# Kernel tuning notes

Measured on AMD Instinct MI355X. Metric: run time of the kernel, lower is better.

## Reference

```python
import jax, jax.numpy as jnp
import numpy as np

THRESH = 1e-5   # replace_denormals threshold
EPS = 1e-5      # instance_norm eps

NUM_LAYERS, TOKEN_LEN, EMBED = 24, 100, 1024
N, B = 1025, 8  # seq (incl. cls token), batch


def _replace_denormals(x):
    return jnp.where((x < THRESH) & (x > -THRESH), THRESH, x)


def _delta_feat(feats, tokens, w_t2f, b_t2f, w_df, b_df, instance_norm):
    # feats: [n, b, c], tokens: [m, c]
    attn = jnp.einsum('nbc,mc->nbm', feats, tokens)
    if instance_norm:  # normalize over m per (n, b), biased variance (torch F.instance_norm)
        mu = attn.mean(axis=-1, keepdims=True)
        var = attn.var(axis=-1, keepdims=True)
        attn = (attn - mu) / jnp.sqrt(var + EPS)
    attn = jax.nn.softmax(attn * (feats.shape[-1] ** -0.5), axis=-1)
    v = tokens[1:] @ w_t2f.T + b_t2f                     # [m-1, c]
    df = jnp.einsum('nbm,mc->nbc', attn[:, :, 1:], v)    # drop first token column
    return (df + feats) @ w_df.T + b_df


def setup_inputs() -> dict:
    key = jax.random.key(0)
    ks = jax.random.split(key, 12)
    C = EMBED
    inp = {
        'feats': jax.random.normal(ks[0], (N, B, C), dtype=jnp.float32),
        'learnable_tokens': jax.random.normal(ks[1], (NUM_LAYERS, TOKEN_LEN, C), dtype=jnp.float32) * 0.04,
        'learnable_tokens2': jax.random.normal(ks[2], (NUM_LAYERS, TOKEN_LEN, C), dtype=jnp.float32) * 0.04,
        'w_t2f': jax.random.normal(ks[3], (C, C), dtype=jnp.float32) * 0.02,
        'b_t2f': jax.random.normal(ks[4], (C,), dtype=jnp.float32) * 0.02,
        'w_df': jax.random.normal(ks[5], (C, C), dtype=jnp.float32) * 0.02,
        'b_df': jax.random.normal(ks[6], (C,), dtype=jnp.float32) * 0.02,
        'w_t2f2': jax.random.normal(ks[7], (C, C), dtype=jnp.float32) * 0.02,
        'b_t2f2': jax.random.normal(ks[8], (C,), dtype=jnp.float32) * 0.02,
        'w_df2': jax.random.normal(ks[9], (C, C), dtype=jnp.float32) * 0.02,
        'b_df2': jax.random.normal(ks[10], (C,), dtype=jnp.float32) * 0.02,
        'scale': jnp.float32(0.001),
        'layer': 0,
    }
    return inp


def reference(feats, learnable_tokens, learnable_tokens2,
              w_t2f, b_t2f, w_df, b_df,
              w_t2f2, b_t2f2, w_df2, b_df2,
              scale, layer):
    # batch_first=False, has_cls_token=True (defaults)
    C = feats.shape[-1]
    cls_tok, x = feats[:1], feats[1:]            # [1,b,c], [n,b,c]
    n, b = x.shape[0], x.shape[1]

    # decompose: fft2 over last two dims (b, c), norm='backward'
    f = jnp.fft.fft2(x)
    re, im = jnp.real(f), jnp.imag(f)
    amp = jnp.sqrt(_replace_denormals(re * re + im * im))
    phase = jnp.arctan2(im, _replace_denormals(re))

    t1 = learnable_tokens[layer]
    t2 = learnable_tokens2[layer]
    d_phase = _delta_feat(phase, t1, w_t2f, b_t2f, w_df, b_df, instance_norm=False)
    d_amp = _delta_feat(amp, t2, w_t2f2, b_t2f2, w_df2, b_df2, instance_norm=True)

    # compose: stacked last dim has size 2, dim 2 has size C -> divide by sqrt(C*2)
    z = (jnp.cos(d_phase) * d_amp + 1j * (jnp.sin(d_phase) * d_amp)) / np.float32(np.sqrt(C * 2.0))
    z = z[..., : C // 2 + 1]                      # torch irfft2 trims last dim to s[-1]//2+1
    delta = jnp.fft.irfft2(z, s=(b, C), norm='ortho')

    out = x + delta * scale
    return jnp.concatenate([cls_tok, out], axis=0)
```

## Files before the change

### kernel.cpp

```cpp
#include <hip/hip_runtime.h>
#include <cstddef>


using bf16x8 = __attribute__((ext_vector_type(8))) short;
using f32x4  = __attribute__((ext_vector_type(4))) float;

__device__ inline short f2bf(float f) {
  union { float f; unsigned u; } v; v.f = f;
  unsigned r = v.u + 0x7FFFu + ((v.u >> 16) & 1u);
  return (short)(r >> 16);
}
__device__ inline float bf2f(short s) {
  union { unsigned u; float f; } v; v.u = ((unsigned)(unsigned short)s) << 16;
  return v.f;
}
__device__ inline void async16(const void* g, void* l) {
  __builtin_amdgcn_global_load_lds(
      (const __attribute__((address_space(1))) void*)g,
      (__attribute__((address_space(3))) void*)l, 16, 0, 0);
}
__device__ inline float fast_atan2(float y, float x) {
  float ax = fabsf(x), ay = fabsf(y);
  float mx = fmaxf(ax, ay), mn = fminf(ax, ay);
  float a = mn * __frcp_rn(mx);
  float s = a * a;
  float r = fmaf(fmaf(fmaf(-0.0464964749f, s, 0.15931422f), s, -0.327622764f),
                 s * a, a);
  if (ay > ax) r = 1.5707963267948966f - r;
  if (x < 0.f) r = 3.14159265358979f - r;
  return (y < 0.f) ? -r : r;
}

__device__ inline int PADi(int i) { return i + (i >> 5); }
__device__ inline int rev4_8(int t) {
  return ((t & 3) << 6) | (((t >> 2) & 3) << 4) | (((t >> 4) & 3) << 2) | ((t >> 6) & 3);
}

__device__ inline void fft8_fwd(float* xr, float* xi) {
  const float r = 0.70710678118654752f;
  float ar[4], ai[4], br[4], bi[4], tr, ti;
  ar[0]=xr[0]+xr[4]; ai[0]=xi[0]+xi[4]; br[0]=xr[0]-xr[4]; bi[0]=xi[0]-xi[4];
  ar[1]=xr[1]+xr[5]; ai[1]=xi[1]+xi[5];
  tr=xr[1]-xr[5]; ti=xi[1]-xi[5]; br[1]=(tr+ti)*r; bi[1]=(ti-tr)*r;
  ar[2]=xr[2]+xr[6]; ai[2]=xi[2]+xi[6];
  tr=xr[2]-xr[6]; ti=xi[2]-xi[6]; br[2]=ti; bi[2]=-tr;
  ar[3]=xr[3]+xr[7]; ai[3]=xi[3]+xi[7];
  tr=xr[3]-xr[7]; ti=xi[3]-xi[7]; br[3]=(ti-tr)*r; bi[3]=-(tr+ti)*r;
  float u0r=ar[0]+ar[2], u0i=ai[0]+ai[2], u1r=ar[1]+ar[3], u1i=ai[1]+ai[3];
  float v0r=ar[0]-ar[2], v0i=ai[0]-ai[2];
  tr=ar[1]-ar[3]; ti=ai[1]-ai[3];
  float v1r=ti, v1i=-tr;
  xr[0]=u0r+u1r; xi[0]=u0i+u1i; xr[4]=u0r-u1r; xi[4]=u0i-u1i;
  xr[2]=v0r+v1r; xi[2]=v0i+v1i; xr[6]=v0r-v1r; xi[6]=v0i-v1i;
  u0r=br[0]+br[2]; u0i=bi[0]+bi[2]; u1r=br[1]+br[3]; u1i=bi[1]+bi[3];
  v0r=br[0]-br[2]; v0i=bi[0]-bi[2];
  tr=br[1]-br[3]; ti=bi[1]-bi[3];
  v1r=ti; v1i=-tr;
  xr[1]=u0r+u1r; xi[1]=u0i+u1i; xr[5]=u0r-u1r; xi[5]=u0i-u1i;
  xr[3]=v0r+v1r; xi[3]=v0i+v1i; xr[7]=v0r-v1r; xi[7]=v0i-v1i;
}
__device__ inline void fft8_inv(float* xr, float* xi) {
  const float r = 0.70710678118654752f;
  float ar[4], ai[4], br[4], bi[4], tr, ti;
  ar[0]=xr[0]+xr[4]; ai[0]=xi[0]+xi[4]; br[0]=xr[0]-xr[4]; bi[0]=xi[0]-xi[4];
  ar[1]=xr[1]+xr[5]; ai[1]=xi[1]+xi[5];
  tr=xr[1]-xr[5]; ti=xi[1]-xi[5]; br[1]=(tr-ti)*r; bi[1]=(tr+ti)*r;
  ar[2]=xr[2]+xr[6]; ai[2]=xi[2]+xi[6];
  tr=xr[2]-xr[6]; ti=xi[2]-xi[6]; br[2]=-ti; bi[2]=tr;
  ar[3]=xr[3]+xr[7]; ai[3]=xi[3]+xi[7];
  tr=xr[3]-xr[7]; ti=xi[3]-xi[7]; br[3]=-(tr+ti)*r; bi[3]=(tr-ti)*r;
  float u0r=ar[0]+ar[2], u0i=ai[0]+ai[2], u1r=ar[1]+ar[3], u1i=ai[1]+ai[3];
  float v0r=ar[0]-ar[2], v0i=ai[0]-ai[2];
  tr=ar[1]-ar[3]; ti=ai[1]-ai[3];
  float v1r=-ti, v1i=tr;
  xr[0]=u0r+u1r; xi[0]=u0i+u1i; xr[4]=u0r-u1r; xi[4]=u0i-u1i;
  xr[2]=v0r+v1r; xi[2]=v0i+v1i; xr[6]=v0r-v1r; xi[6]=v0i-v1i;
  u0r=br[0]+br[2]; u0i=bi[0]+bi[2]; u1r=br[1]+br[3]; u1i=bi[1]+bi[3];
  v0r=br[0]-br[2]; v0i=bi[0]-bi[2];
  tr=br[1]-br[3]; ti=bi[1]-bi[3];
  v1r=-ti; v1i=tr;
  xr[1]=u0r+u1r; xi[1]=u0i+u1i; xr[5]=u0r-u1r; xi[5]=u0i-u1i;
  xr[3]=v0r+v1r; xi[3]=v0i+v1i; xr[7]=v0r-v1r; xi[7]=v0i-v1i;
}

template <int SIGN, int NP>
__device__ inline void fft1024xN(float2 (*zb)[1056], int t) {
#pragma unroll
  for (int s = 0; s < 5; ++s) {
    const int Q = 256 >> (2 * s);
    const int j = t & (Q - 1);
    const int i0 = ((t & ~(Q - 1)) << 2) + j;
    const float ang = (float)SIGN * 6.283185307179586f * (float)j / (float)(4 * Q);
    float s1, c1; __sincosf(ang, &s1, &c1);
    const float c2 = c1 * c1 - s1 * s1, s2 = 2.f * c1 * s1;
    const float c3 = c2 * c1 - s2 * s1, s3 = c2 * s1 + s2 * c1;
#pragma unroll
    for (int p = 0; p < NP; ++p) {
      float2* z = zb[p];
      float2 x0 = z[PADi(i0)];
      float2 x1 = z[PADi(i0 + Q)];
      float2 x2 = z[PADi(i0 + 2 * Q)];
      float2 x3 = z[PADi(i0 + 3 * Q)];
      float t0x = x0.x + x2.x, t0y = x0.y + x2.y;
      float t1x = x0.x - x2.x, t1y = x0.y - x2.y;
      float t2x = x1.x + x3.x, t2y = x1.y + x3.y;
      float t3x = x1.x - x3.x, t3y = x1.y - x3.y;
      float u0x = t0x + t2x, u0y = t0y + t2y;
      float u2x = t0x - t2x, u2y = t0y - t2y;
      float u1x, u1y, u3x, u3y;
      if (SIGN < 0) { u1x = t1x + t3y; u1y = t1y - t3x; u3x = t1x - t3y; u3y = t1y + t3x; }
      else          { u1x = t1x - t3y; u1y = t1y + t3x; u3x = t1x + t3y; u3y = t1y - t3x; }
      z[PADi(i0)]         = make_float2(u0x, u0y);
      z[PADi(i0 + Q)]     = make_float2(u1x * c1 - u1y * s1, u1x * s1 + u1y * c1);
      z[PADi(i0 + 2 * Q)] = make_float2(u2x * c2 - u2y * s2, u2x * s2 + u2y * c2);
      z[PADi(i0 + 3 * Q)] = make_float2(u3x * c3 - u3y * s3, u3x * s3 + u3y * c3);
    }
    __syncthreads();
  }
}

__global__ __launch_bounds__(256) void fwd_fft2_amp_conv(
    const float* __restrict__ feats,
    short* __restrict__ ampb, short* __restrict__ phaseb,
    const float* __restrict__ w1, const float* __restrict__ w2,
    const float* __restrict__ w3, const float* __restrict__ w4,
    const float* __restrict__ lt1, const float* __restrict__ lt2,
    const int* __restrict__ layerp,
    short* __restrict__ Wdst, short* __restrict__ Tdst,
    float* __restrict__ out) {
  if (blockIdx.x >= 1024) {
    const int id = blockIdx.x - 1024;
    const int t4 = threadIdx.x * 4;
    if (id < 4096) {
      const int z = id >> 10, row = id & 1023;
      const float* W = (z == 0 ? w1 : z == 1 ? w2 : z == 2 ? w3 : w4)
                       + (size_t)row * 1024;
      short* D = Wdst + ((size_t)z * 1024 + row) * 1024;
      float4 v = *(const float4*)(W + t4);
      D[t4] = f2bf(v.x); D[t4 + 1] = f2bf(v.y); D[t4 + 2] = f2bf(v.z); D[t4 + 3] = f2bf(v.w);
    } else if (id < 4608) {
      const int i2 = id - 4096;
      const int zz = i2 >> 7, row = i2 & 127;
      const int z = zz & 1, shift = zz >> 1;
      short* D = Tdst + ((size_t)zz * 128 + row) * 1024;
      if (row + shift < 100) {
        const float* S = (z ? lt2 : lt1) + (size_t)layerp[0] * 102400
                         + (size_t)(row + shift) * 1024;
        float4 v = *(const float4*)(S + t4);
        D[t4] = f2bf(v.x); D[t4 + 1] = f2bf(v.y); D[t4 + 2] = f2bf(v.z); D[t4 + 3] = f2bf(v.w);
      } else {
        D[t4] = 0; D[t4 + 1] = 0; D[t4 + 2] = 0; D[t4 + 3] = 0;
      }
    } else {
      const int i = (id - 4608) * 256 + threadIdx.x;
      out[i] = feats[i];
    }
    return;
  }
  __shared__ float2 zb[4][1056];
  const int t = threadIdx.x;
  const int n = blockIdx.x;
  const float* base = feats + 8192 + (size_t)n * 8192;
#pragma unroll
  for (int p = 0; p < 4; ++p) {
    const float* x0 = base + (size_t)(2 * p) * 1024;
    const float* x1 = x0 + 1024;
#pragma unroll
    for (int m = 0; m < 4; ++m) {
      const int c = t + 256 * m;
      zb[p][PADi(c)] = make_float2(x0[c], x1[c]);
    }
  }
  __syncthreads();
  fft1024xN<-1, 4>(zb, t);
  const int rt = rev4_8(t);
  short* ab = ampb + (size_t)n * 8192;
  short* pb = phaseb + (size_t)n * 8192;
#pragma unroll
  for (int m = 0; m < 4; ++m) {
    const int k = 256 * m + t;
    const int kk = (1024 - k) & 1023;
    const int pos  = 4 * rt + m;
    const int pos2 = 4 * rev4_8(kk & 255) + (kk >> 8);
    float xr[8], xi[8];
#pragma unroll
    for (int p = 0; p < 4; ++p) {
      float2 Z = zb[p][PADi(pos)];
      float2 W = zb[p][PADi(pos2)];
      xr[2 * p]     = 0.5f * (Z.x + W.x);
      xi[2 * p]     = 0.5f * (Z.y - W.y);
      xr[2 * p + 1] = 0.5f * (Z.y + W.y);
      xi[2 * p + 1] = 0.5f * (W.x - Z.x);
    }
    fft8_fwd(xr, xi);
#pragma unroll
    for (int kb = 0; kb < 8; ++kb) {
      float sr = xr[kb], si = xi[kb];
      float r2 = sr * sr + si * si;
      if (r2 < 1e-5f) r2 = 1e-5f;
      float a = sqrtf(r2);
      float rr = (sr < 1e-5f && sr > -1e-5f) ? 1e-5f : sr;
      float ph = fast_atan2(si, rr);
      ab[kb * 1024 + k] = f2bf(a);
      pb[kb * 1024 + k] = f2bf(ph);
    }
  }
}

__global__ __launch_bounds__(256) void gemm_sm_v(
    const short* A0, const short* A1,
    const short* Tok,
    const short* Wall,
    const float* bt1, const float* bt2,
    short* __restrict__ awb,
    short* __restrict__ vrow) {
  __shared__ __align__(16) char smem[39040];
  const int z = blockIdx.z;
  const int tid = threadIdx.x;
  const int wave = tid >> 6, lane = tid & 63;
  const int m16 = lane & 15, quad = lane >> 4;
  const int fcol = ((quad ^ ((m16 >> 1) & 3)) * 8) + m16 * 32;
  const int r0 = tid >> 2;
  const int csw = (((tid & 3) ^ ((r0 >> 1) & 3)) * 8);

  if (blockIdx.x >= 256) {
    const int jb = blockIdx.x - 256;
    const short* A = Tok + (size_t)(2 + z) * 128 * 1024;
    const short* B = Wall + (size_t)z * 1024 * 1024;
    const float* bias = z ? bt2 : bt1;
    short* C = vrow + (size_t)z * 128 * 1024;
    const int K = 1024;
    short* As = (short*)smem;
    short* Bs = (short*)(smem + 8192);
    const int wm = (wave & 1) * 64, wn = (wave >> 1) * 64;
    f32x4 acc[4][4];
#pragma unroll
    for (int i = 0; i < 4; ++i)
#pragma unroll
      for (int j = 0; j < 4; ++j) acc[i][j] = (f32x4){0.f, 0.f, 0.f, 0.f};
    const short* aSrc0 = A + (size_t)r0 * K + csw;
    const short* aSrc1 = aSrc0 + (size_t)64 * K;
    const short* bSrc0 = B + (size_t)(jb * 128 + r0) * K + csw;
    const short* bSrc1 = bSrc0 + (size_t)64 * K;
    short* aDst0 = As + tid * 8;
    short* aDst1 = As + 2048 + tid * 8;
    short* bDst0 = Bs + tid * 8;
    short* bDst1 = Bs + 2048 + tid * 8;
    for (int k0 = 0; k0 < K; k0 += 32) {
      async16(aSrc0 + k0, aDst0);
      async16(aSrc1 + k0, aDst1);
      async16(bSrc0 + k0, bDst0);
      async16(bSrc1 + k0, bDst1);
      __syncthreads();
      bf16x8 af[4], bg[4];
#pragma unroll
      for (int ib = 0; ib < 4; ++ib)
        af[ib] = *(const bf16x8*)(As + (wm + ib * 16) * 32 + fcol);
#pragma unroll
      for (int jb2 = 0; jb2 < 4; ++jb2)
        bg[jb2] = *(const bf16x8*)(Bs + (wn + jb2 * 16) * 32 + fcol);
#pragma unroll
      for (int ib = 0; ib < 4; ++ib)
#pragma unroll
        for (int jb2 = 0; jb2 < 4; ++jb2)
          acc[ib][jb2] = __builtin_amdgcn_mfma_f32_16x16x32_bf16(af[ib], bg[jb2], acc[ib][jb2], 0, 0, 0);
      __syncthreads();
    }
#pragma unroll
    for (int ib = 0; ib < 4; ++ib) {
      const int rowb = wm + ib * 16 + quad * 4;
#pragma unroll
      for (int jb2 = 0; jb2 < 4; ++jb2) {
        const int col = jb * 128 + wn + jb2 * 16 + m16;
        const float bcv = bias[col];
#pragma unroll
        for (int r = 0; r < 4; ++r)
          C[(size_t)(rowb + r) * 1024 + col] = f2bf(acc[ib][jb2][r] + bcv);
      }
    }
    return;
  }

  const short* A = z ? A1 : A0;
  const short* B = Tok + (size_t)z * 128 * 1024;
  const int K = 1024;
  short* As = (short*)smem;
  short* Bs = (short*)(smem + 4096);
  float (*ltile)[129] = (float(*)[129])(smem + 20480);
  float (*red1)[8] = (float(*)[8])(smem + 36992);
  float (*red2)[8] = (float(*)[8])(smem + 38016);
  const int wm = (wave & 1) * 16, wn = (wave >> 1) * 64;
  f32x4 acc[4];
#pragma unroll
  for (int j = 0; j < 4; ++j) acc[j] = (f32x4){0.f, 0.f, 0.f, 0.f};
  const int asub = tid >> 7, aidx = tid & 127;
  const int ar0 = aidx >> 2;
  const int acsw = (((aidx & 3) ^ ((ar0 >> 1) & 3)) * 8);
  const short* aSrc = A + (size_t)(blockIdx.x * 32 + ar0) * K + acsw + asub * 32;
  short* aDst = As + asub * 1024 + aidx * 8;
  const short* bSrc0 = B + (size_t)r0 * K + csw;
  const short* bSrc1 = bSrc0 + (size_t)64 * K;
  short* bDst00 = Bs + tid * 8;
  short* bDst01 = Bs + 2048 + tid * 8;
  short* bDst10 = Bs + 4096 + tid * 8;
  short* bDst11 = Bs + 4096 + 2048 + tid * 8;
  for (int k0 = 0; k0 < K; k0 += 64) {
    async16(aSrc + k0, aDst);
    async16(bSrc0 + k0, bDst00);
    async16(bSrc1 + k0, bDst01);
    async16(bSrc0 + k0 + 32, bDst10);
    async16(bSrc1 + k0 + 32, bDst11);
    __syncthreads();
#pragma unroll
    for (int sub = 0; sub < 2; ++sub) {
      bf16x8 af = *(const bf16x8*)(As + sub * 1024 + wm * 32 + fcol);
      bf16x8 bg[4];
#pragma unroll
      for (int jb = 0; jb < 4; ++jb)
        bg[jb] = *(const bf16x8*)(Bs + sub * 4096 + (wn + jb * 16) * 32 + fcol);
#pragma unroll
      for (int jb = 0; jb < 4; ++jb)
        acc[jb] = __builtin_amdgcn_mfma_f32_16x16x32_bf16(af, bg[jb], acc[jb], 0, 0, 0);
    }
    __syncthreads();
  }
#pragma unroll
  for (int jb = 0; jb < 4; ++jb)
#pragma unroll
    for (int r = 0; r < 4; ++r)
      ltile[wm + quad * 4 + r][wn + jb * 16 + m16] = acc[jb][r];
  __syncthreads();
  const int row = tid >> 3, l8 = tid & 7;
  float s = 0.f, q = 0.f;
  for (int c = l8; c < 100; c += 8) { float x = ltile[row][c]; s += x; q += x * x; }
  red1[row][l8] = s; red2[row][l8] = q;
  __syncthreads();
  float ssum = 0.f, qsum = 0.f;
#pragma unroll
  for (int i = 0; i < 8; ++i) { ssum += red1[row][i]; qsum += red2[row][i]; }
  __syncthreads();
  const float mu = ssum * 0.01f;
  const float rinv = rsqrtf(fmaxf(qsum * 0.01f - mu * mu, 0.f) + 1e-5f);
  float mx = -3.4e38f;
  for (int c = l8; c < 100; c += 8) {
    float x = ltile[row][c];
    if (z == 1) x = (x - mu) * rinv;
    x *= 0.03125f;
    ltile[row][c] = x;
    mx = fmaxf(mx, x);
  }
  red1[row][l8] = mx;
  __syncthreads();
#pragma unroll
  for (int i = 0; i < 8; ++i) mx = fmaxf(mx, red1[row][i]);
  __syncthreads();
  float es = 0.f;
  for (int c = l8; c < 100; c += 8) {
    float e = __expf(ltile[row][c] - mx);
    ltile[row][c] = e; es += e;
  }
  red1[row][l8] = es;
  __syncthreads();
  float tot = 0.f;
#pragma unroll
  for (int i = 0; i < 8; ++i) tot += red1[row][i];
  const float inv = 1.f / tot;
  short* Aout = awb + ((size_t)z * 8192 + (size_t)blockIdx.x * 32 + row) * 128;
  for (int c = l8; c < 100; c += 8)
    if (c >= 1) Aout[c - 1] = f2bf(ltile[row][c] * inv);
  for (int k = l8; k < 128; k += 8)
    if (k >= 99) Aout[k] = 0;
}

__global__ __launch_bounds__(256) void gemm64(
    const short* A0, const short* A1,
    const short* B0, const short* B1,
    void* C0v, void* C1v, int K, int ldc) {
  const int z = blockIdx.z;
  const short* A = z ? A1 : A0;
  const short* B = z ? B1 : B0;
  void* Cv = z ? C1v : C0v;
  __shared__ __align__(16) short As[64 * 32];
  __shared__ __align__(16) short Bs[128 * 32];
  const int tid = threadIdx.x;
  const int wave = tid >> 6, lane = tid & 63;
  const int m16 = lane & 15, quad = lane >> 4;
  const int wm = (wave & 1) * 32, wn = (wave >> 1) * 64;
  f32x4 acc[2][4];
#pragma unroll
  for (int i = 0; i < 2; ++i)
#pragma unroll
    for (int j = 0; j < 4; ++j) acc[i][j] = (f32x4){0.f, 0.f, 0.f, 0.f};
  const int r0 = tid >> 2;
  const int csw = (((tid & 3) ^ ((r0 >> 1) & 3)) * 8);
  const short* aSrc  = A + (size_t)(blockIdx.x * 64 + r0) * K + csw;
  const short* bSrc0 = B + (size_t)r0 * K + csw;
  const short* bSrc1 = bSrc0 + (size_t)64 * K;
  short* aDst  = As + tid * 8;
  short* bDst0 = Bs + tid * 8;
  short* bDst1 = Bs + 2048 + tid * 8;
  const int fcol = ((quad ^ ((m16 >> 1) & 3)) * 8) + m16 * 32;
  for (int k0 = 0; k0 < K; k0 += 32) {
    async16(aSrc + k0, aDst);
    async16(bSrc0 + k0, bDst0);
    async16(bSrc1 + k0, bDst1);
    __syncthreads();
    bf16x8 af[2], bg[4];
#pragma unroll
    for (int ib = 0; ib < 2; ++ib)
      af[ib] = *(const bf16x8*)(As + (wm + ib * 16) * 32 + fcol);
#pragma unroll
    for (int jb = 0; jb < 4; ++jb)
      bg[jb] = *(const bf16x8*)(Bs + (wn + jb * 16) * 32 + fcol);
#pragma unroll
    for (int ib = 0; ib < 2; ++ib)
#pragma unroll
      for (int jb = 0; jb < 4; ++jb)
        acc[ib][jb] = __builtin_amdgcn_mfma_f32_16x16x32_bf16(af[ib], bg[jb], acc[ib][jb], 0, 0, 0);
    __syncthreads();
  }
#pragma unroll
  for (int ib = 0; ib < 2; ++ib) {
    const int rowb = blockIdx.x * 64 + wm + ib * 16 + quad * 4;
#pragma unroll
    for (int jb = 0; jb < 4; ++jb) {
      const int col = wn + jb * 16 + m16;
#pragma unroll
      for (int r = 0; r < 4; ++r)
        ((short*)Cv)[(size_t)(rowb + r) * ldc + col] = f2bf(acc[ib][jb][r]);
    }
  }
}

#define DUAL_STEP(VM, DOISS)                                                 \
  do {                                                                       \
    asm volatile("s_waitcnt vmcnt(" #VM ")" ::: "memory");                   \
    __builtin_amdgcn_s_barrier();                                            \
    if (DOISS) {                                                             \
      const int kp = k + 3;                                                  \
      short* ad = &As[kp & 3][0];                                            \
      short* bd = &Bs[kp & 3][0];                                            \
      const short *as0, *as1, *bs0, *bs1;                                    \
      if (kp < NS1) {                                                        \
        const int c = kp << 5;                                               \
        as0 = A1 + aO1_0 + c; as1 = A1 + aO1_1 + c;                          \
        bs0 = B1 + bO1_0 + c; bs1 = B1 + bO1_1 + c;                          \
      } else {                                                               \
        const int c = (kp - NS1) << 5;                                       \
        as0 = A2 + aO2_0 + c; as1 = A2 + aO2_1 + c;                          \
        bs0 = B2 + bO2_0 + c; bs1 = B2 + bO2_1 + c;                          \
      }                                                                      \
      async16(as0, ad + tid * 8);                                            \
      async16(as1, ad + 4096 + tid * 8);                                     \
      async16(bs0, bd + tid * 8);                                            \
      async16(bs1, bd + 4096 + tid * 8);                                     \
    }                                                                        \
    {                                                                        \
      const short* Asl = &As[k & 3][0];                                      \
      const short* Bsl = &Bs[k & 3][0];                                      \
      bf16x8 bg[4], af[4];                                                   \
      _Pragma("unroll")                                                      \
      for (int jb = 0; jb < 4; ++jb)                                         \
        bg[jb] = *(const bf16x8*)(Bsl + (wn + jb * 16) * 32 + fcol);         \
      _Pragma("unroll")                                                      \
      for (int ib = 0; ib < 4; ++ib)                                         \
        af[ib] = *(const bf16x8*)(Asl + (wm + ib * 16) * 32 + fcol);         \
      _Pragma("unroll")                                                      \
      for (int ib = 0; ib < 4; ++ib)                                         \
        _Pragma("unroll")                                                    \
        for (int jb = 0; jb < 4; ++jb)                                       \
          acc[ib][jb] = __builtin_amdgcn_mfma_f32_16x16x32_bf16(             \
              af[ib], bg[jb], acc[ib][jb], 0, 0, 0);                         \
      _Pragma("unroll")                                                      \
      for (int ib = 0; ib < 4; ++ib)                                         \
        af[ib] = *(const bf16x8*)(Asl + (wm + 64 + ib * 16) * 32 + fcol);    \
      _Pragma("unroll")                                                      \
      for (int ib = 0; ib < 4; ++ib)                                         \
        _Pragma("unroll")                                                    \
        for (int jb = 0; jb < 4; ++jb)                                       \
          acc[ib + 4][jb] = __builtin_amdgcn_mfma_f32_16x16x32_bf16(         \
              af[ib], bg[jb], acc[ib + 4][jb], 0, 0, 0);                     \
    }                                                                        \
    __builtin_amdgcn_sched_barrier(0);                                       \
  } while (0)

__global__ __launch_bounds__(512) void gemm256_dual(
    const short* A1_0, const short* A1_1,
    const short* B1_0, const short* B1_1,
    const short* A2_0, const short* A2_1,
    const short* B2_0, const short* B2_1,
    const float* bias0, const float* bias1,
    short* C0, short* C1, int K1, int K2, int ldc) {
  const int z = blockIdx.z;
  const short* A1 = z ? A1_1 : A1_0;
  const short* B1 = z ? B1_1 : B1_0;
  const short* A2 = z ? A2_1 : A2_0;
  const short* B2 = z ? B2_1 : B2_0;
  const float* bias = z ? bias1 : bias0;
  short* C = z ? C1 : C0;
  __shared__ __align__(16) short As[4][8192];
  __shared__ __align__(16) short Bs[4][8192];
  const int tid = threadIdx.x;
  const int wave = tid >> 6, lane = tid & 63;
  const int m16 = lane & 15, quad = lane >> 4;
  const int wm = (wave & 1) * 128, wn = (wave >> 1) * 64;
  const int fcol = ((quad ^ ((m16 >> 1) & 3)) * 8) + m16 * 32;
  const int r0 = tid >> 2;
  const int csw = (((tid & 3) ^ ((r0 >> 1) & 3)) * 8);
  const size_t aO1_0 = (size_t)(blockIdx.x * 256 + r0) * (size_t)K1 + csw;
  const size_t aO1_1 = aO1_0 + (size_t)128 * K1;
  const size_t bO1_0 = (size_t)(blockIdx.y * 256 + r0) * (size_t)K1 + csw;
  const size_t bO1_1 = bO1_0 + (size_t)128 * K1;
  const size_t aO2_0 = (size_t)(blockIdx.x * 256 + r0) * (size_t)K2 + csw;
  const size_t aO2_1 = aO2_0 + (size_t)128 * K2;
  const size_t bO2_0 = (size_t)(blockIdx.y * 256 + r0) * (size_t)K2 + csw;
  const size_t bO2_1 = bO2_0 + (size_t)128 * K2;
  const int NS1 = K1 >> 5;
  const int NT  = NS1 + (K2 >> 5);
  f32x4 acc[8][4];
#pragma unroll
  for (int i = 0; i < 8; ++i)
#pragma unroll
    for (int j = 0; j < 4; ++j) acc[i][j] = (f32x4){0.f, 0.f, 0.f, 0.f};
#pragma unroll
  for (int k = 0; k < 3; ++k) {
    short* ad = &As[k & 3][0];
    short* bd = &Bs[k & 3][0];
    const short *as0, *as1, *bs0, *bs1;
    if (k < NS1) {
      const int c = k << 5;
      as0 = A1 + aO1_0 + c; as1 = A1 + aO1_1 + c;
      bs0 = B1 + bO1_0 + c; bs1 = B1 + bO1_1 + c;
    } else {
      const int c = (k - NS1) << 5;
      as0 = A2 + aO2_0 + c; as1 = A2 + aO2_1 + c;
      bs0 = B2 + bO2_0 + c; bs1 = B2 + bO2_1 + c;
    }
    async16(as0, ad + tid * 8);
    async16(as1, ad + 4096 + tid * 8);
    async16(bs0, bd + tid * 8);
    async16(bs1, bd + 4096 + tid * 8);
  }
#pragma unroll 1
  for (int k = 0; k < NT - 2; ++k) {
    DUAL_STEP(8, (k + 3 < NT));
  }
  { const int k = NT - 2; DUAL_STEP(4, false); }
  { const int k = NT - 1; DUAL_STEP(0, false); }
#pragma unroll
  for (int ib = 0; ib < 8; ++ib) {
    const int rowb = blockIdx.x * 256 + wm + ib * 16 + quad * 4;
#pragma unroll
    for (int jb = 0; jb < 4; ++jb) {
      const int col = blockIdx.y * 256 + wn + jb * 16 + m16;
      const float bcv = bias[col];
#pragma unroll
      for (int r = 0; r < 4; ++r) {
        const size_t idx = (size_t)(rowb + r) * (size_t)ldc + col;
        C[idx] = f2bf(acc[ib][jb][r] + bcv);
      }
    }
  }
}
#undef DUAL_STEP

__global__ __launch_bounds__(256) void inv_fft2_res(const short* __restrict__ dPb,
                                                    const short* __restrict__ dAb,
                                                    const float* __restrict__ feats,
                                                    const float* __restrict__ scalep,
                                                    float* __restrict__ out) {
  __shared__ float2 zb[2][1056];
  const int t = threadIdx.x;
  const int n = blockIdx.x >> 1, q = blockIdx.x & 1;
  const short* pp = dPb + (size_t)n * 8192;
  const short* ap = dAb + (size_t)n * 8192;
  const float invs = 0.022097086912079608f;
  const float inv8 = 0.35355339059327373f;
  for (int k = t; k < 513; k += 256) {
    float zr[8], zi[8];
#pragma unroll
    for (int b = 0; b < 8; ++b) {
      float p = bf2f(pp[b * 1024 + k]);
      float a = bf2f(ap[b * 1024 + k]) * invs;
      float s, c; __sincosf(p, &s, &c);
      zr[b] = c * a; zi[b] = s * a;
    }
    fft8_inv(zr, zi);
#pragma unroll
    for (int l = 0; l < 2; ++l) {
      const int bp = 4 * q + 2 * l;
      float ax = zr[bp] * inv8,     ay = zi[bp] * inv8;
      float bx = zr[bp + 1] * inv8, by = zi[bp + 1] * inv8;
      zb[l][PADi(k)] = make_float2(ax - by, ay + bx);
      if (k >= 1 && k <= 511)
        zb[l][PADi(1024 - k)] = make_float2(ax + by, bx - ay);
    }
  }
  __syncthreads();
  fft1024xN<1, 2>(zb, t);
  const int rt = rev4_8(t);
  const float s = scalep[0] * 0.03125f;
#pragma unroll
  for (int l = 0; l < 2; ++l) {
    const int p4 = 2 * q + l;
    const size_t ob0 = 8192 + ((size_t)n * 8 + 2 * p4) * 1024;
    const size_t ob1 = ob0 + 1024;
#pragma unroll
    for (int m = 0; m < 4; ++m) {
      const int nn = 256 * m + t;
      float2 y = zb[l][PADi(4 * rt + m)];
      out[ob0 + nn] = feats[ob0 + nn] + y.x * s;
      out[ob1 + nn] = feats[ob1 + nn] + y.y * s;
    }
  }
}

extern "C" void kernel_launch(void* const* d_in, const int* in_sizes, int n_in,
                              void* d_out, int out_size, void* d_ws, size_t ws_size,
                              hipStream_t stream) {
  const float* feats  = (const float*)d_in[0];
  const float* lt1    = (const float*)d_in[1];
  const float* lt2    = (const float*)d_in[2];
  const float* w_t2f  = (const float*)d_in[3];
  const float* b_t2f  = (const float*)d_in[4];
  const float* w_df   = (const float*)d_in[5];
  const float* b_df   = (const float*)d_in[6];
  const float* w_t2f2 = (const float*)d_in[7];
  const float* b_t2f2 = (const float*)d_in[8];
  const float* w_df2  = (const float*)d_in[9];
  const float* b_df2  = (const float*)d_in[10];
  const float* scalep = (const float*)d_in[11];
  const int*   layerp = (const int*)d_in[12];
  float* out = (float*)d_out;
  (void)in_sizes; (void)n_in; (void)out_size; (void)ws_size;

  const size_t SZ = 8192ull * 1024ull;
  short* Pa   = (short*)d_ws;
  short* Pb   = Pa + SZ;
  short* awb  = Pb + SZ;
  short* Tok  = awb + 2ull * 8192 * 128;
  short* Wall = Tok + 4ull * 128 * 1024;
  short* vrow = Wall + 4ull * 1024 * 1024;
  short* V2T  = vrow + 2ull * 128 * 1024;
  short* dP   = V2T + 2ull * 1024 * 128;
  short* dA   = dP + SZ;

  fwd_fft2_amp_conv<<<dim3(5664), dim3(256), 0, stream>>>(
      feats, Pb, Pa, w_t2f, w_t2f2, w_df, w_df2, lt1, lt2, layerp,
      Wall, Tok, out);
  gemm_sm_v<<<dim3(264, 1, 2), dim3(256), 0, stream>>>(
      Pa, Pb, Tok, Wall, b_t2f, b_t2f2, awb, vrow);
  gemm64<<<dim3(16, 1, 2), dim3(256), 0, stream>>>(
      Wall + 2 * 1024 * 1024, Wall + 3 * 1024 * 1024,
      vrow, vrow + 128 * 1024,
      V2T, V2T + 1024 * 128, 1024, 128);
  gemm256_dual<<<dim3(32, 4, 2), dim3(512), 0, stream>>>(
      awb, awb + 8192 * 128, V2T, V2T + 1024 * 128,
      Pa, Pb, Wall + 2 * 1024 * 1024, Wall + 3 * 1024 * 1024,
      b_df, b_df2, dP, dA, 128, 1024, 1024);
  inv_fft2_res<<<dim3(2048), dim3(256), 0, stream>>>(dP, dA, feats, scalep, out);
}
```

Baseline: 256.8 us.

## Restructure dual GEMM main loop into ping-pong phases with setprio and split loads

The 256x256 dual GEMM K-loop is reorganized into two phases per K-step. Each phase issues LDS fragment reads and half of the async global->LDS prefetches, then hits a barrier and runs a prioritized MFMA block bracketed by s_setprio. The vmcnt wait moves to the end of each step and the loop peeling is adjusted. The aim is to interleave memory issue with MFMA work across waves, in exchange for extra barriers per step and a riskier wait-count schedule.

New measurement: 255.1 us. Within noise of the previous version (-0.7%).

```diff
diff --git a/kernel.cpp b/kernel.cpp
--- a/kernel.cpp
+++ b/kernel.cpp
@@ -432,15 +432,15 @@
   }
 }
 
-#define DUAL_STEP(VM, DOISS)                                                 \
+#define SLOT8(VM, DOSTAGE)                                                   \
   do {                                                                       \
-    asm volatile("s_waitcnt vmcnt(" #VM ")" ::: "memory");                   \
-    __builtin_amdgcn_s_barrier();                                            \
-    if (DOISS) {                                                             \
-      const int kp = k + 3;                                                  \
-      short* ad = &As[kp & 3][0];                                            \
-      short* bd = &Bs[kp & 3][0];                                            \
-      const short *as0, *as1, *bs0, *bs1;                                    \
+    const short* Asl = &As[k & 3][0];                                        \
+    const short* Bsl = &Bs[k & 3][0];                                        \
+    const int kp = k + 3;                                                    \
+    const short *as0 = nullptr, *as1 = nullptr, *bs0 = nullptr, *bs1 = nullptr; \
+    short *ad = nullptr, *bd = nullptr;                                      \
+    if (DOSTAGE) {                                                           \
+      ad = &As[kp & 3][0]; bd = &Bs[kp & 3][0];                              \
       if (kp < NS1) {                                                        \
         const int c = kp << 5;                                               \
         as0 = A1 + aO1_0 + c; as1 = A1 + aO1_1 + c;                          \
@@ -450,38 +450,54 @@
         as0 = A2 + aO2_0 + c; as1 = A2 + aO2_1 + c;                          \
         bs0 = B2 + bO2_0 + c; bs1 = B2 + bO2_1 + c;                          \
       }                                                                      \
+    }                                                                        \
+    bf16x8 bg[4], af[4];                                                     \
+       \
+    _Pragma("unroll")                                                        \
+    for (int jb = 0; jb < 4; ++jb)                                           \
+      bg[jb] = *(const bf16x8*)(Bsl + (wn + jb * 16) * 32 + fcol);           \
+    _Pragma("unroll")                                                        \
+    for (int ib = 0; ib < 4; ++ib)                                           \
+      af[ib] = *(const bf16x8*)(Asl + (wm + ib * 16) * 32 + fcol);           \
+    if (DOSTAGE) {                                                           \
       async16(as0, ad + tid * 8);                                            \
       async16(as1, ad + 4096 + tid * 8);                                     \
+    }                                                                        \
+    __builtin_amdgcn_sched_barrier(0);                                       \
+    __builtin_amdgcn_s_barrier();                                            \
+    asm volatile("s_waitcnt lgkmcnt(0)" ::: "memory");                       \
+    __builtin_amdgcn_s_setprio(1);                                           \
+    _Pragma("unroll")                                                        \
+    for (int ib = 0; ib < 4; ++ib)                                           \
+      _Pragma("unroll")                                                      \
+      for (int jb = 0; jb < 4; ++jb)                                         \
+        acc[ib][jb] = __builtin_amdgcn_mfma_f32_16x16x32_bf16(               \
+            af[ib], bg[jb], acc[ib][jb], 0, 0, 0);                           \
+    __builtin_amdgcn_s_setprio(0);                                           \
+    __builtin_amdgcn_sched_barrier(0);                                       \
+    __builtin_amdgcn_s_barrier();                                            \
+        \
+    _Pragma("unroll")                                                        \
+    for (int ib = 0; ib < 4; ++ib)                                           \
+      af[ib] = *(const bf16x8*)(Asl + (wm + 64 + ib * 16) * 32 + fcol);      \
+    if (DOSTAGE) {                                                           \
       async16(bs0, bd + tid * 8);                                            \
       async16(bs1, bd + 4096 + tid * 8);                                     \
     }                                                                        \
-    {                                                                        \
-      const short* Asl = &As[k & 3][0];                                      \
-      const short* Bsl = &Bs[k & 3][0];                                      \
-      bf16x8 bg[4], af[4];                                                   \
+    __builtin_amdgcn_sched_barrier(0);                                       \
+    __builtin_amdgcn_s_barrier();                                            \
+    asm volatile("s_waitcnt lgkmcnt(0)" ::: "memory");                       \
+    __builtin_amdgcn_s_setprio(1);                                           \
+    _Pragma("unroll")                                                        \
+    for (int ib = 0; ib < 4; ++ib)                                           \
       _Pragma("unroll")                                                      \
       for (int jb = 0; jb < 4; ++jb)                                         \
-        bg[jb] = *(const bf16x8*)(Bsl + (wn + jb * 16) * 32 + fcol);         \
-      _Pragma("unroll")                                                      \
-      for (int ib = 0; ib < 4; ++ib)                                         \
-        af[ib] = *(const bf16x8*)(Asl + (wm + ib * 16) * 32 + fcol);         \
-      _Pragma("unroll")                                                      \
-      for (int ib = 0; ib < 4; ++ib)                                         \
-        _Pragma("unroll")                                                    \
-        for (int jb = 0; jb < 4; ++jb)                                       \
-          acc[ib][jb] = __builtin_amdgcn_mfma_f32_16x16x32_bf16(             \
-              af[ib], bg[jb], acc[ib][jb], 0, 0, 0);                         \
-      _Pragma("unroll")                                                      \
-      for (int ib = 0; ib < 4; ++ib)                                         \
-        af[ib] = *(const bf16x8*)(Asl + (wm + 64 + ib * 16) * 32 + fcol);    \
-      _Pragma("unroll")                                                      \
-      for (int ib = 0; ib < 4; ++ib)                                         \
-        _Pragma("unroll")                                                    \
-        for (int jb = 0; jb < 4; ++jb)                                       \
-          acc[ib + 4][jb] = __builtin_amdgcn_mfma_f32_16x16x32_bf16(         \
-              af[ib], bg[jb], acc[ib + 4][jb], 0, 0, 0);                     \
-    }                                                                        \
+        acc[ib + 4][jb] = __builtin_amdgcn_mfma_f32_16x16x32_bf16(           \
+            af[ib], bg[jb], acc[ib + 4][jb], 0, 0, 0);                       \
+    __builtin_amdgcn_s_setprio(0);                                           \
+    asm volatile("s_waitcnt vmcnt(" #VM ")" ::: "memory");                   \
     __builtin_amdgcn_sched_barrier(0);                                       \
+    __builtin_amdgcn_s_barrier();                                            \
   } while (0)
 
 __global__ __launch_bounds__(512) void gemm256_dual(
@@ -541,12 +557,16 @@
     async16(bs0, bd + tid * 8);
     async16(bs1, bd + 4096 + tid * 8);
   }
+  asm volatile("s_waitcnt vmcnt(8)" ::: "memory");
+  __builtin_amdgcn_sched_barrier(0);
+  __builtin_amdgcn_s_barrier();
 #pragma unroll 1
-  for (int k = 0; k < NT - 2; ++k) {
-    DUAL_STEP(8, (k + 3 < NT));
-  }
-  { const int k = NT - 2; DUAL_STEP(4, false); }
-  { const int k = NT - 1; DUAL_STEP(0, false); }
+  for (int k = 0; k < NT - 3; ++k) {
+    SLOT8(8, true);
+  }
+  { const int k = NT - 3; SLOT8(4, false); }
+  { const int k = NT - 2; SLOT8(0, false); }
+  { const int k = NT - 1; SLOT8(0, false); }
 #pragma unroll
   for (int ib = 0; ib < 8; ++ib) {
     const int rowb = blockIdx.x * 256 + wm + ib * 16 + quad * 4;
@@ -562,7 +582,7 @@
     }
   }
 }
-#undef DUAL_STEP
+#undef SLOT8
 
 __global__ __launch_bounds__(256) void inv_fft2_res(const short* __restrict__ dPb,
                                                     const short* __restrict__ dAb,
```
